# Performance work log

Hardware: AMD Instinct MI355X
Metric: run time of the kernel (lower is better)

## Reference

```python
import jax, jax.numpy as jnp
import numpy as np

N = 100_000      # n_nodes
E = 1_000_000    # n_edges (avg degree 10)
DIN = 64
DOUT = 64


def setup_inputs() -> dict:
    key = jax.random.key(0)
    k1, k2, k3, k4 = jax.random.split(key, 4)
    x = jax.random.normal(k1, (N, DIN), dtype=jnp.float32)
    edge_index = jax.random.randint(k2, (2, E), 0, N, dtype=jnp.int32)
    # GCNConv linear weight (glorot-ish scale) and bias
    W = jax.random.normal(k3, (DIN, DOUT), dtype=jnp.float32) * (1.0 / np.sqrt(DIN))
    b = jax.random.normal(k4, (DOUT,), dtype=jnp.float32) * 0.01
    return {"x": x, "edge_index": edge_index, "W": W, "b": b}


def reference(x, edge_index, W, b):
    n = x.shape[0]
    # linear transform first (PyG GCNConv: x = self.lin(x))
    h = x @ W  # [N, DOUT]
    # add self-loops
    loop = jnp.arange(n, dtype=edge_index.dtype)
    row = jnp.concatenate([edge_index[0], loop])  # source j
    col = jnp.concatenate([edge_index[1], loop])  # target i
    # symmetric normalization: deg computed on target index (PyG gcn_norm)
    deg = jax.ops.segment_sum(jnp.ones(row.shape[0], dtype=h.dtype), col, num_segments=n)
    dinv = jnp.where(deg > 0, jax.lax.rsqrt(deg), 0.0)
    norm = dinv[row] * dinv[col]  # [E+N]
    # gather source features, scale, scatter-add to targets
    out = jax.ops.segment_sum(norm[:, None] * h[row], col, num_segments=n)
    out = out + b
    # dropout is identity in eval mode; act = relu
    return jax.nn.relu(out)
```

## Files before the change

kernel.cpp:

```cpp
#include <hip/hip_runtime.h>
#include <hip/hip_bf16.h>

#define F 64
#define BK 64
#define CAP 1024
#define ECAP 1024
#define KMAX 1600
#define PA_BLOCKS 512

typedef __attribute__((ext_vector_type(8))) short bf16x8;
typedef __attribute__((ext_vector_type(4))) float f32x4;

static __device__ inline short f2bf_bits(float f) {
    union { __hip_bfloat16 b; short s; } cv;
    cv.b = __float2bfloat16(f);
    return cv.s;
}

static __device__ inline float bf_lo(unsigned u) { return __uint_as_float(u << 16); }
static __device__ inline float bf_hi(unsigned u) { return __uint_as_float(u & 0xffff0000u); }

struct Acc8 {
    float a0, a1, a2, a3, a4, a5, a6, a7;
    __device__ inline void fma8(float wt, uint4 hv) {
        a0 += wt * bf_lo(hv.x);
        a1 += wt * bf_hi(hv.x);
        a2 += wt * bf_lo(hv.y);
        a3 += wt * bf_hi(hv.y);
        a4 += wt * bf_lo(hv.z);
        a5 += wt * bf_hi(hv.z);
        a6 += wt * bf_lo(hv.w);
        a7 += wt * bf_hi(hv.w);
    }
};

__global__ void __launch_bounds__(256)
k1_kernel(const float* __restrict__ x, const float* __restrict__ W,
          __hip_bfloat16* __restrict__ h,
          const int* __restrict__ row, const int* __restrict__ col,
          int* __restrict__ bcursor, unsigned* __restrict__ bin,
          int n, int e, int ngemm, int K, int chunk) {
    __shared__ int smem[2 * KMAX];
    int tid = threadIdx.x;

    if ((int)blockIdx.x < ngemm) {
        short* Wb = (short*)smem;
        for (int i = tid; i < F * F; i += 256) Wb[i] = f2bf_bits(W[i]);
        __syncthreads();
        int lane = tid & 63;
        int wv = tid >> 6;
        int quad = lane >> 4;
        int l16 = lane & 15;

        bf16x8 bfr[2][4];
#pragma unroll
        for (int ks = 0; ks < 2; ++ks)
#pragma unroll
            for (int nb = 0; nb < 4; ++nb) {
                bf16x8 f;
#pragma unroll
                for (int j = 0; j < 8; ++j)
                    f[j] = Wb[(ks * 32 + quad * 8 + j) * F + nb * 16 + l16];
                bfr[ks][nb] = f;
            }

        int blockbase = blockIdx.x * 128;
#pragma unroll
        for (int mt = 0; mt < 2; ++mt) {
            int trow = blockbase + (wv * 2 + mt) * 16;
            int ar = trow + l16;
            bf16x8 af0, af1;
            if (ar < n) {
                const float* xr = x + (size_t)ar * F + quad * 8;
                float4 v0 = ((const float4*)xr)[0];
                float4 v1 = ((const float4*)xr)[1];
                float4 v2 = ((const float4*)(xr + 32))[0];
                float4 v3 = ((const float4*)(xr + 32))[1];
                af0[0] = f2bf_bits(v0.x); af0[1] = f2bf_bits(v0.y);
                af0[2] = f2bf_bits(v0.z); af0[3] = f2bf_bits(v0.w);
                af0[4] = f2bf_bits(v1.x); af0[5] = f2bf_bits(v1.y);
                af0[6] = f2bf_bits(v1.z); af0[7] = f2bf_bits(v1.w);
                af1[0] = f2bf_bits(v2.x); af1[1] = f2bf_bits(v2.y);
                af1[2] = f2bf_bits(v2.z); af1[3] = f2bf_bits(v2.w);
                af1[4] = f2bf_bits(v3.x); af1[5] = f2bf_bits(v3.y);
                af1[6] = f2bf_bits(v3.z); af1[7] = f2bf_bits(v3.w);
            } else {
                af0 = (bf16x8)0; af1 = (bf16x8)0;
            }
            f32x4 acc[4];
#pragma unroll
            for (int nb = 0; nb < 4; ++nb) {
                acc[nb] = (f32x4)0.f;
                acc[nb] = __builtin_amdgcn_mfma_f32_16x16x32_bf16(af0, bfr[0][nb], acc[nb], 0, 0, 0);
                acc[nb] = __builtin_amdgcn_mfma_f32_16x16x32_bf16(af1, bfr[1][nb], acc[nb], 0, 0, 0);
            }
#pragma unroll
            for (int nb = 0; nb < 4; ++nb)
#pragma unroll
                for (int r = 0; r < 4; ++r) {
                    int grow = trow + quad * 4 + r;
                    if (grow < n)
                        h[(size_t)grow * F + nb * 16 + l16] = __float2bfloat16(acc[nb][r]);
                }
        }
    } else {
        int* lh = smem;
        int* lbase = smem + KMAX;
        int pb = blockIdx.x - ngemm;
        int s = pb * chunk;
        int lim = min(s + chunk, e);
        for (int i = tid; i < K; i += 256) lh[i] = 0;
        __syncthreads();
        for (int i = s + tid; i < lim; i += 256) atomicAdd(&lh[col[i] >> 6], 1);
        __syncthreads();
        for (int i = tid; i < K; i += 256) {
            int c = lh[i];
            lbase[i] = c ? atomicAdd(&bcursor[i], c) : 0;
            lh[i] = 0;
        }
        __syncthreads();
        for (int i = s + tid; i < lim; i += 256) {
            int d = col[i];
            int bkt = d >> 6;
            int off = lbase[bkt] + atomicAdd(&lh[bkt], 1);
            if (off < CAP)
                bin[(size_t)bkt * CAP + off] = ((unsigned)row[i] << 6) | ((unsigned)d & 63u);
        }
    }
}

__global__ void __launch_bounds__(256)
dinv_kernel(const unsigned* __restrict__ bin, const int* __restrict__ bcursor,
            float* __restrict__ dinv, int n) {
    __shared__ int lcnt[BK];
    int tid = threadIdx.x;
    int b = blockIdx.x;
    int s = b * CAP;
    int cnt = min(bcursor[b], ECAP);
    if (tid < BK) lcnt[tid] = 0;
    __syncthreads();
    for (int p = tid; p < cnt; p += 256) atomicAdd(&lcnt[bin[s + p] & 63u], 1);
    __syncthreads();
    if (tid < BK) {
        int node = (b << 6) + tid;
        if (node < n) dinv[node] = rsqrtf((float)(lcnt[tid] + 1));
    }
}

__global__ void __launch_bounds__(256)
gather_kernel(const unsigned* __restrict__ bin, const int* __restrict__ bcursor,
              const float* __restrict__ dinv, const __hip_bfloat16* __restrict__ h,
              const float* __restrict__ bias, float* __restrict__ out, int n) {
    __shared__ unsigned ebuf[ECAP];
    __shared__ uint2 sent[ECAP];
    __shared__ int lcnt[BK];
    __shared__ int sstart[BK];
    __shared__ int lcur[BK];
    __shared__ int sc[BK];
    __shared__ float sdinv[BK];
    int tid = threadIdx.x;
    int b = blockIdx.x;
    int base = b << 6;
    int s = b * CAP;
    int cnt = min(bcursor[b], ECAP);

    if (tid < BK) lcnt[tid] = 0;
    __syncthreads();
    for (int p = tid; p < cnt; p += 256) {
        unsigned u = bin[s + p];
        ebuf[p] = u;
        atomicAdd(&lcnt[u & 63u], 1);
    }
    __syncthreads();
    if (tid < BK) sc[tid] = lcnt[tid];
    __syncthreads();
    for (int off = 1; off < BK; off <<= 1) {
        int t = (tid < BK && tid >= off) ? sc[tid - off] : 0;
        __syncthreads();
        if (tid < BK) sc[tid] += t;
        __syncthreads();
    }
    if (tid < BK) {
        int c = lcnt[tid];
        int st = sc[tid] - c;
        sstart[tid] = st;
        lcur[tid] = st;
        sdinv[tid] = rsqrtf((float)(c + 1));
    }
    __syncthreads();
    for (int p = tid; p < cnt; p += 256) {
        unsigned u = ebuf[p];
        int src = (int)(u >> 6);
        float w = dinv[src];
        int pos = atomicAdd(&lcur[u & 63u], 1);
        sent[pos] = make_uint2((unsigned)src, __float_as_uint(w));
    }
    __syncthreads();

    int g = tid >> 3, cl = tid & 7;
    const uint4* h8 = (const uint4*)h;
#pragma unroll
    for (int r = 0; r < 2; ++r) {
        int ln = r * 32 + g;
        int node = base + ln;
        if (node >= n) continue;
        float di = sdinv[ln];
        Acc8 ac = {0.f, 0.f, 0.f, 0.f, 0.f, 0.f, 0.f, 0.f};
        {
            uint4 hv = h8[(size_t)node * 8 + cl];
            ac.fma8(di, hv);
        }
        int p = sstart[ln];
        int pend = p + lcnt[ln];
        for (; p + 4 <= pend; p += 4) {
            uint2 e0 = sent[p];
            uint2 e1 = sent[p + 1];
            uint2 e2 = sent[p + 2];
            uint2 e3 = sent[p + 3];
            uint4 v0 = h8[(size_t)e0.x * 8 + cl];
            uint4 v1 = h8[(size_t)e1.x * 8 + cl];
            uint4 v2 = h8[(size_t)e2.x * 8 + cl];
            uint4 v3 = h8[(size_t)e3.x * 8 + cl];
            ac.fma8(__uint_as_float(e0.y), v0);
            ac.fma8(__uint_as_float(e1.y), v1);
            ac.fma8(__uint_as_float(e2.y), v2);
            ac.fma8(__uint_as_float(e3.y), v3);
        }
        for (; p < pend; ++p) {
            uint2 ew = sent[p];
            uint4 hv = h8[(size_t)ew.x * 8 + cl];
            ac.fma8(__uint_as_float(ew.y), hv);
        }
        float4 b0 = ((const float4*)bias)[cl * 2];
        float4 b1 = ((const float4*)bias)[cl * 2 + 1];
        float4 r0, r1;
        r0.x = di * ac.a0 + b0.x; r0.y = di * ac.a1 + b0.y;
        r0.z = di * ac.a2 + b0.z; r0.w = di * ac.a3 + b0.w;
        r1.x = di * ac.a4 + b1.x; r1.y = di * ac.a5 + b1.y;
        r1.z = di * ac.a6 + b1.z; r1.w = di * ac.a7 + b1.w;
        r0.x = r0.x > 0.f ? r0.x : 0.f; r0.y = r0.y > 0.f ? r0.y : 0.f;
        r0.z = r0.z > 0.f ? r0.z : 0.f; r0.w = r0.w > 0.f ? r0.w : 0.f;
        r1.x = r1.x > 0.f ? r1.x : 0.f; r1.y = r1.y > 0.f ? r1.y : 0.f;
        r1.z = r1.z > 0.f ? r1.z : 0.f; r1.w = r1.w > 0.f ? r1.w : 0.f;
        ((float4*)out)[(size_t)node * 16 + cl * 2] = r0;
        ((float4*)out)[(size_t)node * 16 + cl * 2 + 1] = r1;
    }
}

extern "C" void kernel_launch(void* const* d_in, const int* in_sizes, int n_in,
                              void* d_out, int out_size, void* d_ws, size_t ws_size,
                              hipStream_t stream) {
    const float* x = (const float*)d_in[0];
    const int* ei  = (const int*)d_in[1];
    const float* W = (const float*)d_in[2];
    const float* b = (const float*)d_in[3];
    float* out = (float*)d_out;

    int n = in_sizes[0] / F;
    int e = in_sizes[1] / 2;
    const int* row = ei;
    const int* col = ei + e;
    int K = (n + BK - 1) / BK;

    __hip_bfloat16* h = (__hip_bfloat16*)d_ws;
    unsigned* bin = (unsigned*)((char*)d_ws + (size_t)n * F * 2);
    float* dinv   = (float*)(bin + (size_t)KMAX * CAP);
    int* bcursor  = (int*)(dinv + n);

    (void)hipMemsetAsync(bcursor, 0, KMAX * sizeof(int), stream);

    int ngemm = (n + 127) / 128;
    int chunk = (e + PA_BLOCKS - 1) / PA_BLOCKS;
    k1_kernel<<<ngemm + PA_BLOCKS, 256, 0, stream>>>(x, W, h, row, col, bcursor,
                                                     bin, n, e, ngemm, K, chunk);

    dinv_kernel<<<K, 256, 0, stream>>>(bin, bcursor, dinv, n);

    gather_kernel<<<K, 256, 0, stream>>>(bin, bcursor, dinv, h, b, out, n);
}
```

Baseline: 135.4 us.

## Stream gathered neighbor rows into LDS via async global_load_lds pipeline

Restructures the gather phase so each wave handles the combined edge span of its 8 nodes in batches of 8 edges. Neighbor feature rows are prefetched three batches ahead with async global-to-LDS loads into a 4-slot ring buffer. Each node-group then reads only its own edges from LDS. The aim is to keep many independent gathers in flight and hide memory latency. The cost is extra LDS use (16 KB), wasted loads on clamped tail positions, and relying on vmcnt ordering for correctness.

Measured after the change: 161.9 us. 19.5% more time.

```diff
diff --git a/kernel.cpp b/kernel.cpp
--- a/kernel.cpp
+++ b/kernel.cpp
@@ -33,6 +33,12 @@
         a7 += wt * bf_hi(hv.w);
     }
 };
+
+static __device__ inline void gload_lds16(const void* g, void* l) {
+    __builtin_amdgcn_global_load_lds(
+        (const __attribute__((address_space(1))) void*)g,
+        (__attribute__((address_space(3))) void*)l, 16, 0, 0);
+}
 
 __global__ void __launch_bounds__(256)
 k1_kernel(const float* __restrict__ x, const float* __restrict__ W,
@@ -153,6 +159,7 @@
               const float* __restrict__ bias, float* __restrict__ out, int n) {
     __shared__ unsigned ebuf[ECAP];
     __shared__ uint2 sent[ECAP];
+    __shared__ uint4 slab[4][256];
     __shared__ int lcnt[BK];
     __shared__ int sstart[BK];
     __shared__ int lcur[BK];
@@ -197,53 +204,73 @@
     }
     __syncthreads();
 
-    int g = tid >> 3, cl = tid & 7;
+    int lane = tid & 63;
+    int wv = tid >> 6;
+    int g = tid >> 3;
+    int cl = tid & 7;
+    int eb = lane >> 3;
     const uint4* h8 = (const uint4*)h;
-#pragma unroll
+    uint4* slw = slab[wv];
+
     for (int r = 0; r < 2; ++r) {
+        int ln0 = r * 32 + wv * 8;
+        int spanS = sstart[ln0];
+        int spanE = sstart[ln0 + 7] + lcnt[ln0 + 7];
+        int len = spanE - spanS;
         int ln = r * 32 + g;
         int node = base + ln;
-        if (node >= n) continue;
         float di = sdinv[ln];
+        int myS = sstart[ln];
+        int myE = myS + lcnt[ln];
         Acc8 ac = {0.f, 0.f, 0.f, 0.f, 0.f, 0.f, 0.f, 0.f};
-        {
+        if (node < n) {
             uint4 hv = h8[(size_t)node * 8 + cl];
             ac.fma8(di, hv);
         }
-        int p = sstart[ln];
-        int pend = p + lcnt[ln];
-        for (; p + 4 <= pend; p += 4) {
-            uint2 e0 = sent[p];
-            uint2 e1 = sent[p + 1];
-            uint2 e2 = sent[p + 2];
-            uint2 e3 = sent[p + 3];
-            uint4 v0 = h8[(size_t)e0.x * 8 + cl];
-            uint4 v1 = h8[(size_t)e1.x * 8 + cl];
-            uint4 v2 = h8[(size_t)e2.x * 8 + cl];
-            uint4 v3 = h8[(size_t)e3.x * 8 + cl];
-            ac.fma8(__uint_as_float(e0.y), v0);
-            ac.fma8(__uint_as_float(e1.y), v1);
-            ac.fma8(__uint_as_float(e2.y), v2);
-            ac.fma8(__uint_as_float(e3.y), v3);
-        }
-        for (; p < pend; ++p) {
-            uint2 ew = sent[p];
-            uint4 hv = h8[(size_t)ew.x * 8 + cl];
-            ac.fma8(__uint_as_float(ew.y), hv);
-        }
-        float4 b0 = ((const float4*)bias)[cl * 2];
-        float4 b1 = ((const float4*)bias)[cl * 2 + 1];
-        float4 r0, r1;
-        r0.x = di * ac.a0 + b0.x; r0.y = di * ac.a1 + b0.y;
-        r0.z = di * ac.a2 + b0.z; r0.w = di * ac.a3 + b0.w;
-        r1.x = di * ac.a4 + b1.x; r1.y = di * ac.a5 + b1.y;
-        r1.z = di * ac.a6 + b1.z; r1.w = di * ac.a7 + b1.w;
-        r0.x = r0.x > 0.f ? r0.x : 0.f; r0.y = r0.y > 0.f ? r0.y : 0.f;
-        r0.z = r0.z > 0.f ? r0.z : 0.f; r0.w = r0.w > 0.f ? r0.w : 0.f;
-        r1.x = r1.x > 0.f ? r1.x : 0.f; r1.y = r1.y > 0.f ? r1.y : 0.f;
-        r1.z = r1.z > 0.f ? r1.z : 0.f; r1.w = r1.w > 0.f ? r1.w : 0.f;
-        ((float4*)out)[(size_t)node * 16 + cl * 2] = r0;
-        ((float4*)out)[(size_t)node * 16 + cl * 2 + 1] = r1;
+        int nb = (len + 7) >> 3;
+        if (nb > 0) {
+            int lastp = spanE - 1;
+            for (int t = 0; t < 3; ++t) {
+                int pos = spanS + t * 8 + eb;
+                pos = pos > lastp ? lastp : pos;
+                unsigned sv = sent[pos].x;
+                gload_lds16(h8 + (size_t)sv * 8 + cl, slw + (t & 3) * 64);
+            }
+            for (int bb = 0; bb < nb; ++bb) {
+                {
+                    int t = bb + 3;
+                    int pos = spanS + t * 8 + eb;
+                    pos = pos > lastp ? lastp : pos;
+                    unsigned sv = sent[pos].x;
+                    gload_lds16(h8 + (size_t)sv * 8 + cl, slw + (t & 3) * 64);
+                }
+                asm volatile("s_waitcnt vmcnt(3)" ::: "memory");
+                __builtin_amdgcn_sched_barrier(0);
+                int q0 = spanS + bb * 8;
+                int qa = myS > q0 ? myS : q0;
+                int qb = myE < q0 + 8 ? myE : q0 + 8;
+                const uint4* sl = slw + (bb & 3) * 64;
+                for (int q = qa; q < qb; ++q) {
+                    float w = __uint_as_float(sent[q].y);
+                    ac.fma8(w, sl[(q - q0) * 8 + cl]);
+                }
+            }
+        }
+        if (node < n) {
+            float4 b0 = ((const float4*)bias)[cl * 2];
+            float4 b1 = ((const float4*)bias)[cl * 2 + 1];
+            float4 r0, r1;
+            r0.x = di * ac.a0 + b0.x; r0.y = di * ac.a1 + b0.y;
+            r0.z = di * ac.a2 + b0.z; r0.w = di * ac.a3 + b0.w;
+            r1.x = di * ac.a4 + b1.x; r1.y = di * ac.a5 + b1.y;
+            r1.z = di * ac.a6 + b1.z; r1.w = di * ac.a7 + b1.w;
+            r0.x = r0.x > 0.f ? r0.x : 0.f; r0.y = r0.y > 0.f ? r0.y : 0.f;
+            r0.z = r0.z > 0.f ? r0.z : 0.f; r0.w = r0.w > 0.f ? r0.w : 0.f;
+            r1.x = r1.x > 0.f ? r1.x : 0.f; r1.y = r1.y > 0.f ? r1.y : 0.f;
+            r1.z = r1.z > 0.f ? r1.z : 0.f; r1.w = r1.w > 0.f ? r1.w : 0.f;
+            ((float4*)out)[(size_t)node * 16 + cl * 2] = r0;
+            ((float4*)out)[(size_t)node * 16 + cl * 2 + 1] = r1;
+        }
     }
 }
 
```
